# Kernel tuning notes

Measured on AMD Instinct MI355X. Metric: run time of the kernel, lower is better.

## Reference

```python
import jax, jax.numpy as jnp
import numpy as np

ENC_DIM = 64

def setup_inputs() -> dict:
    key = jax.random.key(0)
    ks = jax.random.split(key, 7)
    B, C, H, W = 16, 64, 128, 128
    s = 1.0 / np.sqrt(C)
    return {
        "x": jax.random.normal(ks[0], (B, C, H, W), jnp.float32),
        "wq_w": jax.random.normal(ks[1], (ENC_DIM, C), jnp.float32) * s,
        "wq_b": jax.random.normal(ks[2], (ENC_DIM,), jnp.float32) * 0.01,
        "wk_w": jax.random.normal(ks[3], (ENC_DIM, C), jnp.float32) * s,
        "wk_b": jax.random.normal(ks[4], (ENC_DIM,), jnp.float32) * 0.01,
        "wv_w": jax.random.normal(ks[5], (ENC_DIM, C), jnp.float32) * s,
        "wv_b": jax.random.normal(ks[6], (ENC_DIM,), jnp.float32) * 0.01,
    }

def _conv1x1(x, w, b):
    # 1x1 conv == per-pixel linear: [B,C,H,W] x [E,C] -> [B,E,H,W]
    return jnp.einsum('bchw,ec->behw', x, w) + b[None, :, None, None]

def reference(x, wq_w, wq_b, wk_w, wk_b, wv_w, wv_b):
    scaler = jnp.sqrt(jnp.asarray(ENC_DIM, x.dtype))
    Q = _conv1x1(x, wq_w, wq_b)  # [B,E,H,W]
    K = _conv1x1(x, wk_w, wk_b)
    V = _conv1x1(x, wv_w, wv_b)
    # scores = Q @ K^T over last two dims -> [B,E,H,H]
    scores = jnp.einsum('behw,bekw->behk', Q, K) / scaler
    temp1 = jax.nn.softmax(scores, axis=-1)          # softmax over last dim; dropout is identity (eval)
    # Q^T @ K -> [B,E,W,W], softmax over dim -2
    t2 = jnp.einsum('behw,behv->bewv', Q, K) / scaler
    temp2 = jax.nn.softmax(t2, axis=-2)
    # temp1 @ V @ temp2 -> [B,E,H,W]
    tv = jnp.einsum('behk,bekw->behw', temp1, V)
    return jnp.einsum('behw,bewv->behv', tv, temp2)
```

## Files before the change

### kernel.cpp

```cpp
#include <hip/hip_runtime.h>
#include <hip/hip_bf16.h>

typedef __attribute__((ext_vector_type(8))) short short8;
typedef __attribute__((ext_vector_type(4))) float f32x4;

#define MFMA16(a, b, c) __builtin_amdgcn_mfma_f32_16x16x32_bf16((a), (b), (c), 0, 0, 0)

__device__ __forceinline__ short f2bf(float f) {
  union { float f; unsigned u; } v; v.f = f;
  unsigned r = v.u + 0x7fffu + ((v.u >> 16) & 1u);
  return (short)(r >> 16);
}
__device__ __forceinline__ unsigned pack2(float lo, float hi) {
  return (unsigned)(unsigned short)f2bf(lo) | ((unsigned)(unsigned short)f2bf(hi) << 16);
}

__global__ __launch_bounds__(256) void qkv_kernel(
    const float* __restrict__ x,
    const float* __restrict__ wq, const float* __restrict__ bq,
    const float* __restrict__ wk, const float* __restrict__ bk,
    const float* __restrict__ wv, const float* __restrict__ bv,
    short* __restrict__ Q, short* __restrict__ K, short* __restrict__ V)
{
  __shared__ alignas(16) short xs[64 * 256];
  __shared__ alignas(16) short ws[3 * 64 * 64];
  __shared__ float bs[3 * 64];

  const int t    = threadIdx.x;
  const int b    = blockIdx.x >> 6;
  const int pt   = blockIdx.x & 63;
  const int pix0 = pt << 8;
  const float* xb = x + ((size_t)b << 20);

  #pragma unroll
  for (int i = 0; i < 16; ++i) {
    int f4 = i * 256 + t;
    int c  = f4 >> 6;
    int p4 = (f4 & 63) << 2;
    const float4 v = *reinterpret_cast<const float4*>(xb + c * 16384 + pix0 + p4);
    short* d = &xs[c * 256 + p4];
    d[0] = f2bf(v.x); d[1] = f2bf(v.y); d[2] = f2bf(v.z); d[3] = f2bf(v.w);
  }
  {
    #pragma unroll
    for (int i = 0; i < 16; ++i) {
      int idx = i * 256 + t;
      int e = idx >> 6, c = idx & 63;
      int d = e * 64 + (c ^ ((e & 7) << 3));
      ws[d]        = f2bf(wq[idx]);
      ws[d + 4096] = f2bf(wk[idx]);
      ws[d + 8192] = f2bf(wv[idx]);
    }
    if (t < 192) bs[t] = (t < 64) ? bq[t] : ((t < 128) ? bk[t - 64] : bv[t - 128]);
  }
  __syncthreads();

  const int lane = t & 63;
  const int wid  = t >> 6;
  const int p0   = wid << 6;
  const int l15  = lane & 15;
  const int lg   = lane >> 4;

  short8 bfrag[4][2];
  #pragma unroll
  for (int nt = 0; nt < 4; ++nt) {
    int pix = p0 + nt * 16 + l15;
    #pragma unroll
    for (int ks = 0; ks < 2; ++ks) {
      int cb = ks * 32 + (lg << 3);
      short8 f;
      #pragma unroll
      for (int j = 0; j < 8; ++j) f[j] = xs[(cb + j) * 256 + pix];
      bfrag[nt][ks] = f;
    }
  }

  #pragma unroll
  for (int m = 0; m < 3; ++m) {
    short* op = (m == 0) ? Q : ((m == 1) ? K : V);
    short8 afrag[4][2];
    #pragma unroll
    for (int mt = 0; mt < 4; ++mt) {
      int e = mt * 16 + l15;
      #pragma unroll
      for (int ks = 0; ks < 2; ++ks) {
        int cb8 = (ks * 4 + lg) ^ (e & 7);
        afrag[mt][ks] = *reinterpret_cast<const short8*>(&ws[m * 4096 + e * 64 + cb8 * 8]);
      }
    }
    #pragma unroll
    for (int mt = 0; mt < 4; ++mt) {
      #pragma unroll
      for (int nt = 0; nt < 4; ++nt) {
        f32x4 acc = {0.f, 0.f, 0.f, 0.f};
        acc = MFMA16(afrag[mt][0], bfrag[nt][0], acc);
        acc = MFMA16(afrag[mt][1], bfrag[nt][1], acc);
        int e_base = mt * 16 + (lg << 2);
        int pix = pix0 + p0 + nt * 16 + l15;
        #pragma unroll
        for (int r = 0; r < 4; ++r) {
          int e = e_base + r;
          float val = acc[r] + bs[m * 64 + e];
          op[(((size_t)b * 64 + e) << 14) + pix] = f2bf(val);
        }
      }
    }
  }
}

__global__ __launch_bounds__(512) void attn_kernel(
    const short* __restrict__ Qg, const short* __restrict__ Kg,
    const short* __restrict__ Vg, float* __restrict__ out)
{
  __shared__ alignas(16) short B1[128 * 128];
  __shared__ alignas(16) short B2[128 * 128];

  const int t = threadIdx.x;
  const size_t base = (size_t)blockIdx.x << 14;

  auto stage = [&](short* dst, const short* src) {
    #pragma unroll
    for (int i = 0; i < 4; ++i) {
      int eb  = i * 512 + t;
      int row = eb >> 4;
      int cb  = eb & 15;
      float4 v = *reinterpret_cast<const float4*>(src + (eb << 3));
      *reinterpret_cast<float4*>(dst + row * 128 + ((cb ^ (row & 15)) << 3)) = v;
    }
  };

  const int w  = t & 127;
  const int rb = (t >> 7) << 5;

  auto colgather = [&](const short* src, unsigned* p) {
    #pragma unroll
    for (int k2 = 0; k2 < 16; ++k2) {
      int r0 = rb + 2 * k2;
      int r1 = r0 + 1;
      unsigned a  = (unsigned short)src[r0 * 128 + (w ^ ((r0 & 15) << 3))];
      unsigned b_ = (unsigned short)src[r1 * 128 + (w ^ ((r1 & 15) << 3))];
      p[k2] = a | (b_ << 16);
    }
  };
  auto t_write = [&](short* dst, const unsigned* p) {
    const int w15 = w & 15;
    #pragma unroll
    for (int k8 = 0; k8 < 4; ++k8) {
      int hb = (rb >> 3) + k8;
      *reinterpret_cast<short8*>(&dst[w * 128 + ((hb ^ w15) << 3)]) =
          *reinterpret_cast<const short8*>(&p[k8 * 4]);
    }
  };

  const int lane = t & 63;
  const int wid  = t >> 6;
  const int m0   = wid << 4;
  const int l15  = lane & 15;
  const int lg   = lane >> 4;

  f32x4 acc[8];

  auto matmul = [&](const short* bufA, const short* bufB) {
    short8 af[4];
    const short* ba[4];
    #pragma unroll
    for (int ks = 0; ks < 4; ++ks) {
      const int xorb = ((ks * 4 + lg) ^ l15) << 3;
      af[ks] = *reinterpret_cast<const short8*>(&bufA[(m0 + l15) * 128 + xorb]);
      ba[ks] = &bufB[l15 * 128 + xorb];
    }
    #pragma unroll
    for (int n = 0; n < 8; ++n) {
      f32x4 a = {0.f, 0.f, 0.f, 0.f};
      #pragma unroll
      for (int ks = 0; ks < 4; ++ks)
        a = MFMA16(af[ks], *reinterpret_cast<const short8*>(ba[ks] + n * 2048), a);
      acc[n] = a;
    }
  };

  auto softmax_pack = [&](unsigned* pk) {
    #pragma unroll
    for (int r = 0; r < 4; ++r) {
      float mx = acc[0][r];
      #pragma unroll
      for (int n = 1; n < 8; ++n) mx = fmaxf(mx, acc[n][r]);
      mx = fmaxf(mx, __shfl_xor(mx, 1));
      mx = fmaxf(mx, __shfl_xor(mx, 2));
      mx = fmaxf(mx, __shfl_xor(mx, 4));
      mx = fmaxf(mx, __shfl_xor(mx, 8));
      float p[8]; float s = 0.f;
      #pragma unroll
      for (int n = 0; n < 8; ++n) { p[n] = __expf((acc[n][r] - mx) * 0.125f); s += p[n]; }
      s += __shfl_xor(s, 1); s += __shfl_xor(s, 2);
      s += __shfl_xor(s, 4); s += __shfl_xor(s, 8);
      float inv = 1.0f / s;
      #pragma unroll
      for (int np = 0; np < 4; ++np)
        pk[r * 4 + np] = pack2(p[2 * np] * inv, p[2 * np + 1] * inv);
    }
  };

  auto store_pk = [&](short* dst, const unsigned* pk) {
    #pragma unroll
    for (int r = 0; r < 4; ++r) {
      int row = m0 + (lg << 2) + r;
      int sw  = (row & 15) << 3;
      short* dr = dst + row * 128;
      #pragma unroll
      for (int np = 0; np < 4; ++np) {
        unsigned v = pk[r * 4 + np];
        int c0 = (2 * np) * 16 + l15;
        dr[c0 ^ sw]        = (short)(v & 0xffff);
        dr[(c0 + 16) ^ sw] = (short)(v >> 16);
      }
    }
  };

  unsigned t1[16], t2[16];

  stage(B1, Qg + base);
  stage(B2, Kg + base);
  __syncthreads();

  matmul(B1, B2);
  softmax_pack(t1);
  unsigned qc[16], kc[16];
  colgather(B1, qc);
  colgather(B2, kc);
  __syncthreads();

  t_write(B1, qc);
  t_write(B2, kc);
  __syncthreads();

  unsigned vc[16];
  {
    const short* Vsrc = Vg + base;
    #pragma unroll
    for (int k2 = 0; k2 < 16; ++k2) {
      unsigned a  = (unsigned short)Vsrc[(rb + 2 * k2) * 128 + w];
      unsigned b_ = (unsigned short)Vsrc[(rb + 2 * k2 + 1) * 128 + w];
      vc[k2] = a | (b_ << 16);
    }
  }
  matmul(B2, B1);
  softmax_pack(t2);
  __syncthreads();

  t_write(B2, vc);
  store_pk(B1, t1);
  __syncthreads();

  matmul(B1, B2);
  {
    unsigned tv[16];
    #pragma unroll
    for (int r = 0; r < 4; ++r)
      #pragma unroll
      for (int np = 0; np < 4; ++np)
        tv[r * 4 + np] = pack2(acc[2 * np][r], acc[2 * np + 1][r]);
    store_pk(B1, tv);
  }
  __syncthreads();

  store_pk(B2, t2);
  __syncthreads();

  float* ob = out + base;
  #pragma unroll
  for (int n = 0; n < 8; ++n) {
    short8 af[4];
    const short* ba[4];
    #pragma unroll
    for (int ks = 0; ks < 4; ++ks) {
      const int xorb = ((ks * 4 + lg) ^ l15) << 3;
      af[ks] = *reinterpret_cast<const short8*>(&B1[(m0 + l15) * 128 + xorb]);
      ba[ks] = &B2[l15 * 128 + xorb];
    }
    f32x4 a = {0.f, 0.f, 0.f, 0.f};
    #pragma unroll
    for (int ks = 0; ks < 4; ++ks)
      a = MFMA16(af[ks], *reinterpret_cast<const short8*>(ba[ks] + n * 2048), a);
    #pragma unroll
    for (int r = 0; r < 4; ++r) {
      int row = m0 + (lg << 2) + r;
      ob[row * 128 + n * 16 + l15] = a[r];
    }
  }
}

extern "C" void kernel_launch(void* const* d_in, const int* in_sizes, int n_in,
                              void* d_out, int out_size, void* d_ws, size_t ws_size,
                              hipStream_t stream) {
  const float* x  = (const float*)d_in[0];
  const float* wq = (const float*)d_in[1];
  const float* bq = (const float*)d_in[2];
  const float* wk = (const float*)d_in[3];
  const float* bk = (const float*)d_in[4];
  const float* wv = (const float*)d_in[5];
  const float* bv = (const float*)d_in[6];

  const size_t N = (size_t)16 * 64 * 128 * 128;
  short* Q = (short*)d_ws;
  short* K = Q + N;
  short* V = K + N;

  qkv_kernel<<<1024, 256, 0, stream>>>(x, wq, bq, wk, bk, wv, bv, Q, K, V);
  attn_kernel<<<1024, 512, 0, stream>>>(Q, K, V, (float*)d_out);
}
```

Measured before the change: 89.96 us.

## Process two attention slices per block with interleaved software pipelining

Each attention block now handles two (b,e) slices using four 128x128 LDS buffers. The stages of the two slices are interleaved so global loads and LDS transposes for one overlap the MFMA matmuls and softmax of the other, and the number of barrier-separated phases per slice drops. The grid is halved. LDS use doubles to 128KB per block, and the many live register arrays may raise register pressure or cause spills, cutting occupancy.

```diff
diff --git a/kernel.cpp b/kernel.cpp
--- a/kernel.cpp
+++ b/kernel.cpp
@@ -112,11 +112,15 @@
     const short* __restrict__ Qg, const short* __restrict__ Kg,
     const short* __restrict__ Vg, float* __restrict__ out)
 {
-  __shared__ alignas(16) short B1[128 * 128];
-  __shared__ alignas(16) short B2[128 * 128];
+  __shared__ alignas(16) short lds[4 * 16384];
+  short* B1 = lds;
+  short* B2 = lds + 16384;
+  short* B3 = lds + 2 * 16384;
+  short* B4 = lds + 3 * 16384;
 
   const int t = threadIdx.x;
-  const size_t base = (size_t)blockIdx.x << 14;
+  const size_t baseX = (size_t)(blockIdx.x << 1) << 14;
+  const size_t baseY = baseX + 16384;
 
   auto stage = [&](short* dst, const short* src) {
     #pragma unroll
@@ -128,6 +132,20 @@
       *reinterpret_cast<float4*>(dst + row * 128 + ((cb ^ (row & 15)) << 3)) = v;
     }
   };
+  auto stage_ld = [&](const short* src, float4* r) {
+    #pragma unroll
+    for (int i = 0; i < 4; ++i)
+      r[i] = *reinterpret_cast<const float4*>(src + ((i * 512 + t) << 3));
+  };
+  auto stage_st = [&](short* dst, const float4* r) {
+    #pragma unroll
+    for (int i = 0; i < 4; ++i) {
+      int eb  = i * 512 + t;
+      int row = eb >> 4;
+      int cb  = eb & 15;
+      *reinterpret_cast<float4*>(dst + row * 128 + ((cb ^ (row & 15)) << 3)) = r[i];
+    }
+  };
 
   const int w  = t & 127;
   const int rb = (t >> 7) << 5;
@@ -151,6 +169,14 @@
           *reinterpret_cast<const short8*>(&p[k8 * 4]);
     }
   };
+  auto vload = [&](const short* Vsrc, unsigned* p) {
+    #pragma unroll
+    for (int k2 = 0; k2 < 16; ++k2) {
+      unsigned a  = (unsigned short)Vsrc[(rb + 2 * k2) * 128 + w];
+      unsigned b_ = (unsigned short)Vsrc[(rb + 2 * k2 + 1) * 128 + w];
+      p[k2] = a | (b_ << 16);
+    }
+  };
 
   const int lane = t & 63;
   const int wid  = t >> 6;
@@ -216,78 +242,96 @@
       }
     }
   };
-
-  unsigned t1[16], t2[16];
-
-  stage(B1, Qg + base);
-  stage(B2, Kg + base);
-  __syncthreads();
-
-  matmul(B1, B2);
-  softmax_pack(t1);
-  unsigned qc[16], kc[16];
-  colgather(B1, qc);
-  colgather(B2, kc);
-  __syncthreads();
-
-  t_write(B1, qc);
-  t_write(B2, kc);
-  __syncthreads();
-
-  unsigned vc[16];
-  {
-    const short* Vsrc = Vg + base;
-    #pragma unroll
-    for (int k2 = 0; k2 < 16; ++k2) {
-      unsigned a  = (unsigned short)Vsrc[(rb + 2 * k2) * 128 + w];
-      unsigned b_ = (unsigned short)Vsrc[(rb + 2 * k2 + 1) * 128 + w];
-      vc[k2] = a | (b_ << 16);
-    }
-  }
-  matmul(B2, B1);
-  softmax_pack(t2);
-  __syncthreads();
-
-  t_write(B2, vc);
-  store_pk(B1, t1);
-  __syncthreads();
-
-  matmul(B1, B2);
-  {
+  auto store_tv = [&](short* dst) {
     unsigned tv[16];
     #pragma unroll
     for (int r = 0; r < 4; ++r)
       #pragma unroll
       for (int np = 0; np < 4; ++np)
         tv[r * 4 + np] = pack2(acc[2 * np][r], acc[2 * np + 1][r]);
-    store_pk(B1, tv);
-  }
-  __syncthreads();
-
-  store_pk(B2, t2);
-  __syncthreads();
-
-  float* ob = out + base;
-  #pragma unroll
-  for (int n = 0; n < 8; ++n) {
-    short8 af[4];
-    const short* ba[4];
-    #pragma unroll
-    for (int ks = 0; ks < 4; ++ks) {
-      const int xorb = ((ks * 4 + lg) ^ l15) << 3;
-      af[ks] = *reinterpret_cast<const short8*>(&B1[(m0 + l15) * 128 + xorb]);
-      ba[ks] = &B2[l15 * 128 + xorb];
-    }
-    f32x4 a = {0.f, 0.f, 0.f, 0.f};
-    #pragma unroll
-    for (int ks = 0; ks < 4; ++ks)
-      a = MFMA16(af[ks], *reinterpret_cast<const short8*>(ba[ks] + n * 2048), a);
-    #pragma unroll
-    for (int r = 0; r < 4; ++r) {
-      int row = m0 + (lg << 2) + r;
-      ob[row * 128 + n * 16 + l15] = a[r];
-    }
-  }
+    store_pk(dst, tv);
+  };
+  auto outmm = [&](const short* bufA, const short* bufB, float* ob) {
+    #pragma unroll
+    for (int n = 0; n < 8; ++n) {
+      short8 af[4];
+      const short* ba[4];
+      #pragma unroll
+      for (int ks = 0; ks < 4; ++ks) {
+        const int xorb = ((ks * 4 + lg) ^ l15) << 3;
+        af[ks] = *reinterpret_cast<const short8*>(&bufA[(m0 + l15) * 128 + xorb]);
+        ba[ks] = &bufB[l15 * 128 + xorb];
+      }
+      f32x4 a = {0.f, 0.f, 0.f, 0.f};
+      #pragma unroll
+      for (int ks = 0; ks < 4; ++ks)
+        a = MFMA16(af[ks], *reinterpret_cast<const short8*>(ba[ks] + n * 2048), a);
+      #pragma unroll
+      for (int r = 0; r < 4; ++r) {
+        int row = m0 + (lg << 2) + r;
+        ob[row * 128 + n * 16 + l15] = a[r];
+      }
+    }
+  };
+
+  unsigned t1X[16], t2X[16], t1Y[16], t2Y[16];
+  unsigned qcX[16], kcX[16], qcY[16], kcY[16], vcX[16], vcY[16];
+
+  stage(B1, Qg + baseX);
+  stage(B2, Kg + baseX);
+  __syncthreads();
+
+  {
+    float4 rq[4], rk[4];
+    stage_ld(Qg + baseY, rq);
+    stage_ld(Kg + baseY, rk);
+    matmul(B1, B2);
+    softmax_pack(t1X);
+    colgather(B1, qcX);
+    colgather(B2, kcX);
+    stage_st(B3, rq);
+    stage_st(B4, rk);
+  }
+  __syncthreads();
+
+  t_write(B1, qcX);
+  t_write(B2, kcX);
+  matmul(B3, B4);
+  softmax_pack(t1Y);
+  colgather(B3, qcY);
+  colgather(B4, kcY);
+  __syncthreads();
+
+  vload(Vg + baseX, vcX);
+  t_write(B3, qcY);
+  t_write(B4, kcY);
+  matmul(B2, B1);
+  softmax_pack(t2X);
+  __syncthreads();
+
+  vload(Vg + baseY, vcY);
+  store_pk(B1, t1X);
+  t_write(B2, vcX);
+  matmul(B4, B3);
+  softmax_pack(t2Y);
+  __syncthreads();
+
+  store_pk(B3, t1Y);
+  t_write(B4, vcY);
+  matmul(B1, B2);
+  store_tv(B1);
+  __syncthreads();
+
+  store_pk(B2, t2X);
+  matmul(B3, B4);
+  store_tv(B3);
+  __syncthreads();
+
+  store_pk(B4, t2Y);
+  outmm(B1, B2, out + baseX);
+  __syncthreads();
+
+  outmm(B3, B4, out + baseY);
 }
 
 extern "C" void kernel_launch(void* const* d_in, const int* in_sizes, int n_in,
@@ -307,5 +351,5 @@
   short* V = K + N;
 
   qkv_kernel<<<1024, 256, 0, stream>>>(x, wq, bq, wk, bk, wv, bv, Q, K, V);
-  attn_kernel<<<1024, 512, 0, stream>>>(Q, K, V, (float*)d_out);
-}
+  attn_kernel<<<512, 512, 0, stream>>>(Q, K, V, (float*)d_out);
+}
```

After: 119.7 us. 33.0% more time.

## Run two staggered attention slices per 1024-thread block for phase overlap

Applied to the files above, without the earlier changes.

Each block of 1024 threads now handles two (b,e) slices, each owning 64 KB of LDS. The second half of the block runs its phases one barrier behind the first, so memory-heavy and MFMA-heavy phases of the two slices overlap. This relies on __syncthreads being hit a matching number of times in divergent branches. It also doubles LDS per block to 128 KB and forces a 1024-thread launch bound, which can cut registers per thread and cause spills.

```diff
diff --git a/kernel.cpp b/kernel.cpp
--- a/kernel.cpp
+++ b/kernel.cpp
@@ -108,20 +108,22 @@
   }
 }
 
-__global__ __launch_bounds__(512) void attn_kernel(
+__global__ __launch_bounds__(1024) void attn_kernel(
     const short* __restrict__ Qg, const short* __restrict__ Kg,
     const short* __restrict__ Vg, float* __restrict__ out)
 {
-  __shared__ alignas(16) short B1[128 * 128];
-  __shared__ alignas(16) short B2[128 * 128];
-
-  const int t = threadIdx.x;
-  const size_t base = (size_t)blockIdx.x << 14;
+  __shared__ alignas(16) short lds[4 * 16384];
+  const int t  = threadIdx.x;
+  const int sl = t >> 9;
+  const int ts = t & 511;
+  short* BA = lds + sl * 32768;
+  short* BB = BA + 16384;
+  const size_t base = (size_t)(2 * blockIdx.x + sl) << 14;
 
   auto stage = [&](short* dst, const short* src) {
     #pragma unroll
     for (int i = 0; i < 4; ++i) {
-      int eb  = i * 512 + t;
+      int eb  = i * 512 + ts;
       int row = eb >> 4;
       int cb  = eb & 15;
       float4 v = *reinterpret_cast<const float4*>(src + (eb << 3));
@@ -129,8 +131,8 @@
     }
   };
 
-  const int w  = t & 127;
-  const int rb = (t >> 7) << 5;
+  const int w  = ts & 127;
+  const int rb = (ts >> 7) << 5;
 
   auto colgather = [&](const short* src, unsigned* p) {
     #pragma unroll
@@ -151,9 +153,17 @@
           *reinterpret_cast<const short8*>(&p[k8 * 4]);
     }
   };
+  auto vload = [&](const short* Vsrc, unsigned* p) {
+    #pragma unroll
+    for (int k2 = 0; k2 < 16; ++k2) {
+      unsigned a  = (unsigned short)Vsrc[(rb + 2 * k2) * 128 + w];
+      unsigned b_ = (unsigned short)Vsrc[(rb + 2 * k2 + 1) * 128 + w];
+      p[k2] = a | (b_ << 16);
+    }
+  };
 
   const int lane = t & 63;
-  const int wid  = t >> 6;
+  const int wid  = (t >> 6) & 7;
   const int m0   = wid << 4;
   const int l15  = lane & 15;
   const int lg   = lane >> 4;
@@ -216,77 +226,70 @@
       }
     }
   };
-
-  unsigned t1[16], t2[16];
-
-  stage(B1, Qg + base);
-  stage(B2, Kg + base);
-  __syncthreads();
-
-  matmul(B1, B2);
-  softmax_pack(t1);
-  unsigned qc[16], kc[16];
-  colgather(B1, qc);
-  colgather(B2, kc);
-  __syncthreads();
-
-  t_write(B1, qc);
-  t_write(B2, kc);
-  __syncthreads();
-
-  unsigned vc[16];
-  {
-    const short* Vsrc = Vg + base;
-    #pragma unroll
-    for (int k2 = 0; k2 < 16; ++k2) {
-      unsigned a  = (unsigned short)Vsrc[(rb + 2 * k2) * 128 + w];
-      unsigned b_ = (unsigned short)Vsrc[(rb + 2 * k2 + 1) * 128 + w];
-      vc[k2] = a | (b_ << 16);
-    }
-  }
-  matmul(B2, B1);
-  softmax_pack(t2);
-  __syncthreads();
-
-  t_write(B2, vc);
-  store_pk(B1, t1);
-  __syncthreads();
-
-  matmul(B1, B2);
-  {
+  auto store_tv = [&](short* dst) {
     unsigned tv[16];
     #pragma unroll
     for (int r = 0; r < 4; ++r)
       #pragma unroll
       for (int np = 0; np < 4; ++np)
         tv[r * 4 + np] = pack2(acc[2 * np][r], acc[2 * np + 1][r]);
-    store_pk(B1, tv);
-  }
-  __syncthreads();
-
-  store_pk(B2, t2);
-  __syncthreads();
-
-  float* ob = out + base;
-  #pragma unroll
-  for (int n = 0; n < 8; ++n) {
-    short8 af[4];
-    const short* ba[4];
-    #pragma unroll
-    for (int ks = 0; ks < 4; ++ks) {
-      const int xorb = ((ks * 4 + lg) ^ l15) << 3;
-      af[ks] = *reinterpret_cast<const short8*>(&B1[(m0 + l15) * 128 + xorb]);
-      ba[ks] = &B2[l15 * 128 + xorb];
-    }
-    f32x4 a = {0.f, 0.f, 0.f, 0.f};
-    #pragma unroll
-    for (int ks = 0; ks < 4; ++ks)
-      a = MFMA16(af[ks], *reinterpret_cast<const short8*>(ba[ks] + n * 2048), a);
-    #pragma unroll
-    for (int r = 0; r < 4; ++r) {
-      int row = m0 + (lg << 2) + r;
-      ob[row * 128 + n * 16 + l15] = a[r];
-    }
+    store_pk(dst, tv);
+  };
+
+  unsigned t1[16], t2[16], qc[16], kc[16], vc[16];
+
+  auto P1 = [&]() { stage(BA, Qg + base); stage(BB, Kg + base); };
+  auto P2 = [&]() {
+    matmul(BA, BB); softmax_pack(t1);
+    colgather(BA, qc); colgather(BB, kc);
+  };
+  auto P3 = [&]() { t_write(BA, qc); t_write(BB, kc); };
+  auto P4 = [&]() { vload(Vg + base, vc); matmul(BB, BA); softmax_pack(t2); };
+  auto P5 = [&]() { store_pk(BA, t1); t_write(BB, vc); };
+  auto P6 = [&]() { matmul(BA, BB); store_tv(BA); };
+  auto P7 = [&]() { store_pk(BB, t2); };
+  auto P8 = [&]() {
+    float* ob = out + base;
+    #pragma unroll
+    for (int n = 0; n < 8; ++n) {
+      short8 af[4];
+      const short* ba[4];
+      #pragma unroll
+      for (int ks = 0; ks < 4; ++ks) {
+        const int xorb = ((ks * 4 + lg) ^ l15) << 3;
+        af[ks] = *reinterpret_cast<const short8*>(&BA[(m0 + l15) * 128 + xorb]);
+        ba[ks] = &BB[l15 * 128 + xorb];
+      }
+      f32x4 a = {0.f, 0.f, 0.f, 0.f};
+      #pragma unroll
+      for (int ks = 0; ks < 4; ++ks)
+        a = MFMA16(af[ks], *reinterpret_cast<const short8*>(ba[ks] + n * 2048), a);
+      #pragma unroll
+      for (int r = 0; r < 4; ++r) {
+        int row = m0 + (lg << 2) + r;
+        ob[row * 128 + n * 16 + l15] = a[r];
+      }
+    }
+  };
+
+  if (sl == 0) {
+    P1(); __syncthreads();
+    P2(); __syncthreads();
+    P3(); __syncthreads();
+    P4(); __syncthreads();
+    P5(); __syncthreads();
+    P6(); __syncthreads();
+    P7(); __syncthreads();
+    P8(); __syncthreads();
+  } else {
+    __syncthreads(); P1();
+    __syncthreads(); P2();
+    __syncthreads(); P3();
+    __syncthreads(); P4();
+    __syncthreads(); P5();
+    __syncthreads(); P6();
+    __syncthreads(); P7();
+    __syncthreads(); P8();
   }
 }
 
@@ -307,5 +310,5 @@
   short* V = K + N;
 
   qkv_kernel<<<1024, 256, 0, stream>>>(x, wq, bq, wk, bk, wv, bv, Q, K, V);
-  attn_kernel<<<1024, 512, 0, stream>>>(Q, K, V, (float*)d_out);
-}
+  attn_kernel<<<512, 1024, 0, stream>>>(Q, K, V, (float*)d_out);
+}
```

Measured after the change: 103.0 us. +14.5%, slower.

## Halve attention block size so each wave computes two 16-row MFMA tiles

Applied to the files above, without the earlier changes.

Shrinks the attention kernel from 512 to 256 threads per block, with each wave now handling 32 rows (two M tiles) instead of 16. Each B-fragment load from LDS is reused across two MFMAs, and staging, column gather and V load loops are doubled per thread. Fewer waves contend for LDS bandwidth and barriers, but per-thread register use roughly doubles (t1/t2/qc/kc/vc arrays now 32 entries), which may limit occupancy. The launch bound requests 2 blocks per CU, though 64KB of LDS per block may constrain that.

```diff
diff --git a/kernel.cpp b/kernel.cpp
--- a/kernel.cpp
+++ b/kernel.cpp
@@ -108,7 +108,7 @@
   }
 }
 
-__global__ __launch_bounds__(512) void attn_kernel(
+__global__ __launch_bounds__(256, 2) void attn_kernel(
     const short* __restrict__ Qg, const short* __restrict__ Kg,
     const short* __restrict__ Vg, float* __restrict__ out)
 {
@@ -120,8 +120,8 @@
 
   auto stage = [&](short* dst, const short* src) {
     #pragma unroll
-    for (int i = 0; i < 4; ++i) {
-      int eb  = i * 512 + t;
+    for (int i = 0; i < 8; ++i) {
+      int eb  = i * 256 + t;
       int row = eb >> 4;
       int cb  = eb & 15;
       float4 v = *reinterpret_cast<const float4*>(src + (eb << 3));
@@ -130,11 +130,11 @@
   };
 
   const int w  = t & 127;
-  const int rb = (t >> 7) << 5;
+  const int rb = (t >> 7) << 6;
 
   auto colgather = [&](const short* src, unsigned* p) {
     #pragma unroll
-    for (int k2 = 0; k2 < 16; ++k2) {
+    for (int k2 = 0; k2 < 32; ++k2) {
       int r0 = rb + 2 * k2;
       int r1 = r0 + 1;
       unsigned a  = (unsigned short)src[r0 * 128 + (w ^ ((r0 & 15) << 3))];
@@ -145,41 +145,54 @@
   auto t_write = [&](short* dst, const unsigned* p) {
     const int w15 = w & 15;
     #pragma unroll
-    for (int k8 = 0; k8 < 4; ++k8) {
+    for (int k8 = 0; k8 < 8; ++k8) {
       int hb = (rb >> 3) + k8;
       *reinterpret_cast<short8*>(&dst[w * 128 + ((hb ^ w15) << 3)]) =
           *reinterpret_cast<const short8*>(&p[k8 * 4]);
     }
   };
+  auto vload = [&](const short* Vsrc, unsigned* p) {
+    #pragma unroll
+    for (int k2 = 0; k2 < 32; ++k2) {
+      unsigned a  = (unsigned short)Vsrc[(rb + 2 * k2) * 128 + w];
+      unsigned b_ = (unsigned short)Vsrc[(rb + 2 * k2 + 1) * 128 + w];
+      p[k2] = a | (b_ << 16);
+    }
+  };
 
   const int lane = t & 63;
   const int wid  = t >> 6;
-  const int m0   = wid << 4;
+  const int m0   = wid << 5;
   const int l15  = lane & 15;
   const int lg   = lane >> 4;
 
-  f32x4 acc[8];
+  f32x4 acc0[8], acc1[8];
 
   auto matmul = [&](const short* bufA, const short* bufB) {
-    short8 af[4];
+    short8 af0[4], af1[4];
     const short* ba[4];
     #pragma unroll
     for (int ks = 0; ks < 4; ++ks) {
       const int xorb = ((ks * 4 + lg) ^ l15) << 3;
-      af[ks] = *reinterpret_cast<const short8*>(&bufA[(m0 + l15) * 128 + xorb]);
+      af0[ks] = *reinterpret_cast<const short8*>(&bufA[(m0 + l15) * 128 + xorb]);
+      af1[ks] = *reinterpret_cast<const short8*>(&bufA[(m0 + 16 + l15) * 128 + xorb]);
       ba[ks] = &bufB[l15 * 128 + xorb];
     }
     #pragma unroll
     for (int n = 0; n < 8; ++n) {
-      f32x4 a = {0.f, 0.f, 0.f, 0.f};
-      #pragma unroll
-      for (int ks = 0; ks < 4; ++ks)
-        a = MFMA16(af[ks], *reinterpret_cast<const short8*>(ba[ks] + n * 2048), a);
-      acc[n] = a;
-    }
-  };
-
-  auto softmax_pack = [&](unsigned* pk) {
+      f32x4 a0 = {0.f, 0.f, 0.f, 0.f};
+      f32x4 a1 = {0.f, 0.f, 0.f, 0.f};
+      #pragma unroll
+      for (int ks = 0; ks < 4; ++ks) {
+        short8 bf = *reinterpret_cast<const short8*>(ba[ks] + n * 2048);
+        a0 = MFMA16(af0[ks], bf, a0);
+        a1 = MFMA16(af1[ks], bf, a1);
+      }
+      acc0[n] = a0; acc1[n] = a1;
+    }
+  };
+
+  auto softmax_pack = [&](f32x4* acc, unsigned* pk) {
     #pragma unroll
     for (int r = 0; r < 4; ++r) {
       float mx = acc[0][r];
@@ -201,10 +214,10 @@
     }
   };
 
-  auto store_pk = [&](short* dst, const unsigned* pk) {
+  auto store_pk = [&](short* dst, const unsigned* pk, int mbase) {
     #pragma unroll
     for (int r = 0; r < 4; ++r) {
-      int row = m0 + (lg << 2) + r;
+      int row = mbase + (lg << 2) + r;
       int sw  = (row & 15) << 3;
       short* dr = dst + row * 128;
       #pragma unroll
@@ -216,16 +229,32 @@
       }
     }
   };
-
-  unsigned t1[16], t2[16];
+  auto store_accs = [&](short* dst) {
+    unsigned tv[16];
+    #pragma unroll
+    for (int r = 0; r < 4; ++r)
+      #pragma unroll
+      for (int np = 0; np < 4; ++np)
+        tv[r * 4 + np] = pack2(acc0[2 * np][r], acc0[2 * np + 1][r]);
+    store_pk(dst, tv, m0);
+    #pragma unroll
+    for (int r = 0; r < 4; ++r)
+      #pragma unroll
+      for (int np = 0; np < 4; ++np)
+        tv[r * 4 + np] = pack2(acc1[2 * np][r], acc1[2 * np + 1][r]);
+    store_pk(dst, tv, m0 + 16);
+  };
+
+  unsigned t1[32], t2[32];
 
   stage(B1, Qg + base);
   stage(B2, Kg + base);
   __syncthreads();
 
   matmul(B1, B2);
-  softmax_pack(t1);
-  unsigned qc[16], kc[16];
+  softmax_pack(acc0, t1);
+  softmax_pack(acc1, t1 + 16);
+  unsigned qc[32], kc[32];
   colgather(B1, qc);
   colgather(B2, kc);
   __syncthreads();
@@ -234,58 +263,53 @@
   t_write(B2, kc);
   __syncthreads();
 
-  unsigned vc[16];
+  unsigned vc[32];
+  vload(Vg + base, vc);
+  matmul(B2, B1);
+  softmax_pack(acc0, t2);
+  softmax_pack(acc1, t2 + 16);
+  __syncthreads();
+
+  t_write(B2, vc);
+  store_pk(B1, t1, m0);
+  store_pk(B1, t1 + 16, m0 + 16);
+  __syncthreads();
+
+  matmul(B1, B2);
+  store_accs(B1);
+  __syncthreads();
+
+  store_pk(B2, t2, m0);
+  store_pk(B2, t2 + 16, m0 + 16);
+  __syncthreads();
+
   {
-    const short* Vsrc = Vg + base;
-    #pragma unroll
-    for (int k2 = 0; k2 < 16; ++k2) {
-      unsigned a  = (unsigned short)Vsrc[(rb + 2 * k2) * 128 + w];
-      unsigned b_ = (unsigned short)Vsrc[(rb + 2 * k2 + 1) * 128 + w];
-      vc[k2] = a | (b_ << 16);
-    }
-  }
-  matmul(B2, B1);
-  softmax_pack(t2);
-  __syncthreads();
-
-  t_write(B2, vc);
-  store_pk(B1, t1);
-  __syncthreads();
-
-  matmul(B1, B2);
-  {
-    unsigned tv[16];
-    #pragma unroll
-    for (int r = 0; r < 4; ++r)
-      #pragma unroll
-      for (int np = 0; np < 4; ++np)
-        tv[r * 4 + np] = pack2(acc[2 * np][r], acc[2 * np + 1][r]);
-    store_pk(B1, tv);
-  }
-  __syncthreads();
-
-  store_pk(B2, t2);
-  __syncthreads();
-
-  float* ob = out + base;
-  #pragma unroll
-  for (int n = 0; n < 8; ++n) {
-    short8 af[4];
+    float* ob = out + base;
+    short8 af0[4], af1[4];
     const short* ba[4];
     #pragma unroll
     for (int ks = 0; ks < 4; ++ks) {
       const int xorb = ((ks * 4 + lg) ^ l15) << 3;
-      af[ks] = *reinterpret_cast<const short8*>(&B1[(m0 + l15) * 128 + xorb]);
+      af0[ks] = *reinterpret_cast<const short8*>(&B1[(m0 + l15) * 128 + xorb]);
+      af1[ks] = *reinterpret_cast<const short8*>(&B1[(m0 + 16 + l15) * 128 + xorb]);
       ba[ks] = &B2[l15 * 128 + xorb];
     }
-    f32x4 a = {0.f, 0.f, 0.f, 0.f};
-    #pragma unroll
-    for (int ks = 0; ks < 4; ++ks)
-      a = MFMA16(af[ks], *reinterpret_cast<const short8*>(ba[ks] + n * 2048), a);
-    #pragma unroll
-    for (int r = 0; r < 4; ++r) {
-      int row = m0 + (lg << 2) + r;
-      ob[row * 128 + n * 16 + l15] = a[r];
+    #pragma unroll
+    for (int n = 0; n < 8; ++n) {
+      f32x4 a0 = {0.f, 0.f, 0.f, 0.f};
+      f32x4 a1 = {0.f, 0.f, 0.f, 0.f};
+      #pragma unroll
+      for (int ks = 0; ks < 4; ++ks) {
+        short8 bf = *reinterpret_cast<const short8*>(ba[ks] + n * 2048);
+        a0 = MFMA16(af0[ks], bf, a0);
+        a1 = MFMA16(af1[ks], bf, a1);
+      }
+      #pragma unroll
+      for (int r = 0; r < 4; ++r) {
+        int row0 = m0 + (lg << 2) + r;
+        ob[row0 * 128 + n * 16 + l15] = a0[r];
+        ob[(row0 + 16) * 128 + n * 16 + l15] = a1[r];
+      }
     }
   }
 }
@@ -307,5 +331,5 @@
   short* V = K + N;
 
   qkv_kernel<<<1024, 256, 0, stream>>>(x, wq, bq, wk, bk, wv, bv, Q, K, V);
-  attn_kernel<<<1024, 512, 0, stream>>>(Q, K, V, (float*)d_out);
-}
+  attn_kernel<<<1024, 256, 0, stream>>>(Q, K, V, (float*)d_out);
+}
```

New measurement: 86.62 us. 1.04x faster.
